# Kernel optimization log

Measured on AMD Instinct MI355X. Metric: run time of the kernel, lower is better.

## Reference

```python
import jax, jax.numpy as jnp
import numpy as np

N_NODES = 50000
N_EDGES = 800000
IN_FEATS = 512
NUM_HEADS = 4
OUT_FEATS = 64
NEG_SLOPE = 0.2


def setup_inputs() -> dict:
    key = jax.random.key(0)
    k1, k2, k3, k4, k5, k6 = jax.random.split(key, 6)
    feat = jax.random.normal(k1, (N_NODES, IN_FEATS), dtype=jnp.float32)
    W = jax.random.normal(k2, (IN_FEATS, NUM_HEADS * OUT_FEATS), dtype=jnp.float32) * (1.0 / np.sqrt(IN_FEATS))
    attn_l = jax.random.normal(k3, (NUM_HEADS, OUT_FEATS), dtype=jnp.float32) * (1.0 / np.sqrt(OUT_FEATS))
    attn_r = jax.random.normal(k4, (NUM_HEADS, OUT_FEATS), dtype=jnp.float32) * (1.0 / np.sqrt(OUT_FEATS))
    src = jax.random.randint(k5, (N_EDGES,), 0, N_NODES, dtype=jnp.int32)
    dst = jax.random.randint(k6, (N_EDGES,), 0, N_NODES, dtype=jnp.int32)
    return {"feat": feat, "W": W, "attn_l": attn_l, "attn_r": attn_r, "src": src, "dst": dst}


def reference(feat, W, attn_l, attn_r, src, dst):
    N = feat.shape[0]
    H, D = attn_l.shape
    # node-wise projection: fc(feat).view(N, H, D)
    ft = (feat @ W).reshape(N, H, D)
    # per-node attention logits
    el = jnp.einsum('nhd,hd->nh', ft, attn_l)  # [N, H]
    er = jnp.einsum('nhd,hd->nh', ft, attn_r)  # [N, H]
    # edge-wise score: leaky_relu(el[u] + er[v])
    e = jax.nn.leaky_relu(el[src] + er[dst], negative_slope=NEG_SLOPE)  # [E, H]
    # segment softmax over incoming edges of each destination node
    e_max = jax.ops.segment_max(e, dst, num_segments=N)  # [N, H]
    e_max = jnp.where(jnp.isfinite(e_max), e_max, 0.0)
    exp_e = jnp.exp(e - e_max[dst])  # [E, H]
    denom = jax.ops.segment_sum(exp_e, dst, num_segments=N)  # [N, H]
    a = exp_e / denom[dst]  # [E, H]
    # weighted message aggregation: sum_u a(u,v) * ft[u]
    msg = ft[src] * a[:, :, None]  # [E, H, D]
    out = jax.ops.segment_sum(msg, dst, num_segments=N)  # [N, H, D]
    return out.reshape(N, H * D)
```

## Files before the change

### kernel.cpp

```cpp
#include <hip/hip_runtime.h>

#define N_NODES 50000
#define N_EDGES 800000
#define IN_F    512
#define NH      4
#define DH      64
#define HD      256
#define NEG     0.2f
#define NB      ((N_NODES + 255) / 256)

typedef __attribute__((ext_vector_type(8))) short bf16x8;
typedef __attribute__((ext_vector_type(4))) float f32x4;

__device__ __forceinline__ unsigned short f2bf(float x) {
    unsigned u = __float_as_uint(x);
    unsigned r = (u + 0x7FFFu + ((u >> 16) & 1u)) >> 16;
    return (unsigned short)r;
}
__device__ __forceinline__ float bf2f(unsigned short b) {
    return __uint_as_float((unsigned)b << 16);
}

__global__ void zero_kernel(int* __restrict__ p, int n) {
    int i = blockIdx.x * blockDim.x + threadIdx.x;
    if (i < n) p[i] = 0;
}

__global__ __launch_bounds__(256) void count_kernel(const int* __restrict__ dst,
                                                    int* __restrict__ counts) {
    int e = blockIdx.x * blockDim.x + threadIdx.x;
    if (e < N_EDGES) atomicAdd(&counts[dst[e]], 1);
}

__global__ __launch_bounds__(256) void wt_kernel(const float* __restrict__ W,
                                                 unsigned short* __restrict__ Wtb) {
    int i = blockIdx.x * blockDim.x + threadIdx.x;
    if (i >= IN_F * HD) return;
    int k = i >> 8;
    int n = i & 255;
    Wtb[(size_t)n * IN_F + k] = f2bf(W[i]);
}

#define LDP 72
__global__ __launch_bounds__(256) void gemm_kernel(const float* __restrict__ A,
                                                   const unsigned short* __restrict__ Wtb,
                                                   unsigned short* __restrict__ Cb) {
    __shared__ short A_s[128][LDP];
    __shared__ short B_s[128][LDP];

    const int tid  = threadIdx.x;
    const int lane = tid & 63;
    const int wave = tid >> 6;
    const int wr   = wave >> 1;
    const int wc   = wave & 1;
    const int lm   = lane & 15;
    const int quad = lane >> 4;
    const int row0 = blockIdx.x * 128;
    const int col0 = blockIdx.y * 128;

    f32x4 acc[4][4] = {};

    for (int kt = 0; kt < IN_F; kt += 64) {
#pragma unroll
        for (int it = 0; it < 4; it++) {
            int gid = it * 256 + tid;
            int row = gid >> 3;
            int c8  = (gid & 7) * 8;
            int grow = row0 + row;
            float4 v0 = make_float4(0.f, 0.f, 0.f, 0.f);
            float4 v1 = v0;
            if (grow < N_NODES) {
                const float* ap = A + (size_t)grow * IN_F + kt + c8;
                v0 = *(const float4*)(ap);
                v1 = *(const float4*)(ap + 4);
            }
            bf16x8 s;
            s[0] = (short)f2bf(v0.x); s[1] = (short)f2bf(v0.y);
            s[2] = (short)f2bf(v0.z); s[3] = (short)f2bf(v0.w);
            s[4] = (short)f2bf(v1.x); s[5] = (short)f2bf(v1.y);
            s[6] = (short)f2bf(v1.z); s[7] = (short)f2bf(v1.w);
            *(bf16x8*)(&A_s[row][c8]) = s;
        }
#pragma unroll
        for (int it = 0; it < 4; it++) {
            int gid = it * 256 + tid;
            int row = gid >> 3;
            int c8  = (gid & 7) * 8;
            *(bf16x8*)(&B_s[row][c8]) =
                *(const bf16x8*)(Wtb + (size_t)(col0 + row) * IN_F + kt + c8);
        }
        __syncthreads();

#pragma unroll
        for (int kk = 0; kk < 64; kk += 32) {
            bf16x8 af[4], bfr[4];
#pragma unroll
            for (int i = 0; i < 4; i++)
                af[i] = *(const bf16x8*)(&A_s[wr * 64 + i * 16 + lm][kk + quad * 8]);
#pragma unroll
            for (int j = 0; j < 4; j++)
                bfr[j] = *(const bf16x8*)(&B_s[wc * 64 + j * 16 + lm][kk + quad * 8]);
#pragma unroll
            for (int i = 0; i < 4; i++)
#pragma unroll
                for (int j = 0; j < 4; j++)
                    acc[i][j] = __builtin_amdgcn_mfma_f32_16x16x32_bf16(
                        af[i], bfr[j], acc[i][j], 0, 0, 0);
        }
        __syncthreads();
    }

#pragma unroll
    for (int i = 0; i < 4; i++) {
#pragma unroll
        for (int j = 0; j < 4; j++) {
            int gcol = col0 + wc * 64 + j * 16 + lm;
#pragma unroll
            for (int r = 0; r < 4; r++) {
                int grow = row0 + wr * 64 + i * 16 + quad * 4 + r;
                if (grow < N_NODES)
                    Cb[(size_t)grow * HD + gcol] = f2bf(acc[i][j][r]);
            }
        }
    }
}

__global__ __launch_bounds__(256) void el_er_kernel(const unsigned short* __restrict__ ftb,
                                                    const float* __restrict__ attn_l,
                                                    const float* __restrict__ attn_r,
                                                    float* __restrict__ el,
                                                    float* __restrict__ er) {
    int n    = (blockIdx.x * blockDim.x + threadIdx.x) >> 6;
    int lane = threadIdx.x & 63;
    if (n >= N_NODES) return;
    int h = lane >> 4;
    int c = lane * 4;

    ushort4 fv = *(const ushort4*)(ftb + (size_t)n * HD + c);
    float4 al = *(const float4*)(attn_l + c);
    float4 ar = *(const float4*)(attn_r + c);
    float f0 = bf2f(fv.x), f1 = bf2f(fv.y), f2 = bf2f(fv.z), f3 = bf2f(fv.w);
    float pl = f0 * al.x + f1 * al.y + f2 * al.z + f3 * al.w;
    float pr = f0 * ar.x + f1 * ar.y + f2 * ar.z + f3 * ar.w;
#pragma unroll
    for (int off = 8; off > 0; off >>= 1) {
        pl += __shfl_down(pl, off);
        pr += __shfl_down(pr, off);
    }
    if ((lane & 15) == 0) {
        el[(size_t)n * NH + h] = pl;
        er[(size_t)n * NH + h] = pr;
    }
}

__global__ __launch_bounds__(256) void partial_kernel(const int* __restrict__ counts,
                                                      int* __restrict__ bsums) {
    __shared__ int red[4];
    int i = blockIdx.x * 256 + threadIdx.x;
    int c = (i < N_NODES) ? counts[i] : 0;
#pragma unroll
    for (int off = 32; off > 0; off >>= 1) c += __shfl_down(c, off);
    if ((threadIdx.x & 63) == 0) red[threadIdx.x >> 6] = c;
    __syncthreads();
    if (threadIdx.x == 0) bsums[blockIdx.x] = red[0] + red[1] + red[2] + red[3];
}

__global__ __launch_bounds__(256) void bscan_kernel(const int* __restrict__ bsums,
                                                    int* __restrict__ boffs) {
    __shared__ int s[256];
    int tid = threadIdx.x;
    s[tid] = (tid < NB) ? bsums[tid] : 0;
    __syncthreads();
    for (int off = 1; off < 256; off <<= 1) {
        int x = s[tid];
        int a = (tid >= off) ? s[tid - off] : 0;
        __syncthreads();
        s[tid] = x + a;
        __syncthreads();
    }
    if (tid < NB) boffs[tid] = (tid > 0) ? s[tid - 1] : 0;
}

__global__ __launch_bounds__(256) void scatter_scan_kernel(const int* __restrict__ counts,
                                                           const int* __restrict__ boffs,
                                                           int* __restrict__ offsets,
                                                           int* __restrict__ cursor) {
    __shared__ int s[256];
    int tid = threadIdx.x;
    int i = blockIdx.x * 256 + tid;
    s[tid] = (i < N_NODES) ? counts[i] : 0;
    __syncthreads();
    for (int off = 1; off < 256; off <<= 1) {
        int x = s[tid];
        int a = (tid >= off) ? s[tid - off] : 0;
        __syncthreads();
        s[tid] = x + a;
        __syncthreads();
    }
    int excl = (tid > 0) ? s[tid - 1] : 0;
    int o = boffs[blockIdx.x] + excl;
    if (i < N_NODES) { offsets[i] = o; cursor[i] = o; }
    if (i == 0) offsets[N_NODES] = N_EDGES;
}

__device__ __forceinline__ float lrelu_exp(float x) {
    float y = (x > 0.f) ? x : NEG * x;
    return __expf(y);
}

__global__ __launch_bounds__(256) void edge_place_kernel(const int* __restrict__ src,
                                                         const int* __restrict__ dst,
                                                         const float* __restrict__ el,
                                                         const float* __restrict__ er,
                                                         int* __restrict__ cursor,
                                                         int* __restrict__ srcs,
                                                         float* __restrict__ w4s) {
    int e = blockIdx.x * blockDim.x + threadIdx.x;
    if (e >= N_EDGES) return;
    int u = src[e], v = dst[e];
    float4 l = *(const float4*)(el + (size_t)u * NH);
    float4 r = *(const float4*)(er + (size_t)v * NH);
    float4 s;
    s.x = lrelu_exp(l.x + r.x);
    s.y = lrelu_exp(l.y + r.y);
    s.z = lrelu_exp(l.z + r.z);
    s.w = lrelu_exp(l.w + r.w);
    int pos = atomicAdd(&cursor[v], 1);
    srcs[pos] = u;
    *(float4*)(w4s + (size_t)pos * NH) = s;
}

__global__ __launch_bounds__(256) void agg_kernel(const unsigned short* __restrict__ ftb,
                                                  const float* __restrict__ w4s,
                                                  const int* __restrict__ srcs,
                                                  const int* __restrict__ offsets,
                                                  float* __restrict__ out) {
    int wv   = (blockIdx.x * blockDim.x + threadIdx.x) >> 6;
    int lane = threadIdx.x & 63;
    if (wv >= N_NODES) return;

    const int beg = offsets[wv];
    const int end = offsets[wv + 1];
    const int h   = lane >> 4;
    const size_t foff = (size_t)lane * 4;

    float4 acc = make_float4(0.f, 0.f, 0.f, 0.f);
    float dsum = 0.f;

    const int n4 = (end - beg) >> 2;
    int u0, u1, u2, u3;
    if (n4 > 0) {
        const int* sp = srcs + beg;
        u0 = sp[0]; u1 = sp[1]; u2 = sp[2]; u3 = sp[3];
        for (int b = 0; b < n4; b++) {
            const int base = beg + b * 4;
            int v0 = 0, v1 = 0, v2 = 0, v3 = 0;
            if (b + 1 < n4) {
                const int* np = srcs + base + 4;
                v0 = np[0]; v1 = np[1]; v2 = np[2]; v3 = np[3];
            }
            ushort4 f0 = *(const ushort4*)(ftb + (size_t)u0 * HD + foff);
            ushort4 f1 = *(const ushort4*)(ftb + (size_t)u1 * HD + foff);
            ushort4 f2 = *(const ushort4*)(ftb + (size_t)u2 * HD + foff);
            ushort4 f3 = *(const ushort4*)(ftb + (size_t)u3 * HD + foff);
            float w0 = w4s[(size_t)(base + 0) * NH + h];
            float w1 = w4s[(size_t)(base + 1) * NH + h];
            float w2 = w4s[(size_t)(base + 2) * NH + h];
            float w3 = w4s[(size_t)(base + 3) * NH + h];
            acc.x += w0 * bf2f(f0.x) + w1 * bf2f(f1.x) + w2 * bf2f(f2.x) + w3 * bf2f(f3.x);
            acc.y += w0 * bf2f(f0.y) + w1 * bf2f(f1.y) + w2 * bf2f(f2.y) + w3 * bf2f(f3.y);
            acc.z += w0 * bf2f(f0.z) + w1 * bf2f(f1.z) + w2 * bf2f(f2.z) + w3 * bf2f(f3.z);
            acc.w += w0 * bf2f(f0.w) + w1 * bf2f(f1.w) + w2 * bf2f(f2.w) + w3 * bf2f(f3.w);
            dsum += (w0 + w1) + (w2 + w3);
            u0 = v0; u1 = v1; u2 = v2; u3 = v3;
        }
    }
    for (int p = beg + n4 * 4; p < end; p++) {
        int u = srcs[p];
        float w = w4s[(size_t)p * NH + h];
        ushort4 f = *(const ushort4*)(ftb + (size_t)u * HD + foff);
        acc.x += w * bf2f(f.x);
        acc.y += w * bf2f(f.y);
        acc.z += w * bf2f(f.z);
        acc.w += w * bf2f(f.w);
        dsum += w;
    }

    float inv = (dsum > 0.f) ? (1.f / dsum) : 0.f;
    acc.x *= inv; acc.y *= inv; acc.z *= inv; acc.w *= inv;
    *(float4*)(out + (size_t)wv * HD + foff) = acc;
}

extern "C" void kernel_launch(void* const* d_in, const int* in_sizes, int n_in,
                              void* d_out, int out_size, void* d_ws, size_t ws_size,
                              hipStream_t stream) {
    const float* feat   = (const float*)d_in[0];
    const float* W      = (const float*)d_in[1];
    const float* attn_l = (const float*)d_in[2];
    const float* attn_r = (const float*)d_in[3];
    const int*   src    = (const int*)d_in[4];
    const int*   dst    = (const int*)d_in[5];
    float* out = (float*)d_out;

    char* p = (char*)d_ws;
    auto alloc = [&](size_t bytes) -> char* {
        char* r = p;
        p += (bytes + 255) & ~(size_t)255;
        return r;
    };
    unsigned short* ftb     = (unsigned short*)alloc((size_t)N_NODES * HD * 2);
    unsigned short* Wtb     = (unsigned short*)alloc((size_t)IN_F * HD * 2);
    float*          el      = (float*)alloc((size_t)N_NODES * NH * 4);
    float*          er      = (float*)alloc((size_t)N_NODES * NH * 4);
    float*          w4s     = (float*)alloc((size_t)N_EDGES * NH * 4);
    int*            srcs    = (int*)alloc((size_t)N_EDGES * 4);
    int*            counts  = (int*)alloc((size_t)N_NODES * 4);
    int*            offsets = (int*)alloc((size_t)(N_NODES + 1) * 4);
    int*            cursor  = (int*)alloc((size_t)N_NODES * 4);
    int*            bsums   = (int*)alloc((size_t)NB * 4);
    int*            boffs   = (int*)alloc((size_t)NB * 4);

    zero_kernel<<<(N_NODES + 255) / 256, 256, 0, stream>>>(counts, N_NODES);
    count_kernel<<<(N_EDGES + 255) / 256, 256, 0, stream>>>(dst, counts);
    wt_kernel<<<(IN_F * HD + 255) / 256, 256, 0, stream>>>(W, Wtb);
    dim3 ggrid((N_NODES + 127) / 128, HD / 128);
    gemm_kernel<<<ggrid, 256, 0, stream>>>(feat, Wtb, ftb);
    el_er_kernel<<<(N_NODES + 3) / 4, 256, 0, stream>>>(ftb, attn_l, attn_r, el, er);
    partial_kernel<<<NB, 256, 0, stream>>>(counts, bsums);
    bscan_kernel<<<1, 256, 0, stream>>>(bsums, boffs);
    scatter_scan_kernel<<<NB, 256, 0, stream>>>(counts, boffs, offsets, cursor);
    edge_place_kernel<<<(N_EDGES + 255) / 256, 256, 0, stream>>>(src, dst, el, er,
                                                                 cursor, srcs, w4s);
    agg_kernel<<<(N_NODES + 3) / 4, 256, 0, stream>>>(ftb, w4s, srcs, offsets, out);
}
```

Baseline: 357.1 us.

## Shrink GEMM row tile to 64 and prefetch next K tile into registers

The GEMM block tile shrinks from 128x128 to 64x128, which doubles the block count to about 1564 blocks so more work is spread across the CUs. It also adds register prefetching: the global loads for the next K slice are issued after the shared-memory barrier and overlap with the current slice's MFMA work. The cost is that each row of W is reread from global memory twice as often, more registers are held per thread for the prefetch buffers, and each wave does less compute per LDS load.

Result: faster. 349.5 us (-2.1%).

```diff
diff --git a/kernel.cpp b/kernel.cpp
--- a/kernel.cpp
+++ b/kernel.cpp
@@ -41,12 +41,13 @@
     Wtb[(size_t)n * IN_F + k] = f2bf(W[i]);
 }
 
-#define LDP 72
+#define LDPA 72
+#define LDPB 72
 __global__ __launch_bounds__(256) void gemm_kernel(const float* __restrict__ A,
                                                    const unsigned short* __restrict__ Wtb,
                                                    unsigned short* __restrict__ Cb) {
-    __shared__ short A_s[128][LDP];
-    __shared__ short B_s[128][LDP];
+    __shared__ short A_s[64][LDPA];
+    __shared__ short B_s[128][LDPB];
 
     const int tid  = threadIdx.x;
     const int lane = tid & 63;
@@ -55,53 +56,70 @@
     const int wc   = wave & 1;
     const int lm   = lane & 15;
     const int quad = lane >> 4;
-    const int row0 = blockIdx.x * 128;
+    const int row0 = blockIdx.x * 64;
     const int col0 = blockIdx.y * 128;
 
-    f32x4 acc[4][4] = {};
+    const int srow = tid >> 3;
+    const int sc8  = (tid & 7) * 8;
+
+    f32x4 acc[2][4] = {};
+    float4 pa[4];
+    bf16x8 pb[4];
+
+#define LOAD_TILES(KT)                                                         \
+    {                                                                          \
+        int g0 = row0 + srow;                                                  \
+        if (g0 < N_NODES) {                                                    \
+            const float* ap = A + (size_t)g0 * IN_F + (KT) + sc8;              \
+            pa[0] = *(const float4*)ap; pa[1] = *(const float4*)(ap + 4);      \
+        } else { pa[0] = pa[1] = make_float4(0.f, 0.f, 0.f, 0.f); }            \
+        int g1 = row0 + 32 + srow;                                             \
+        if (g1 < N_NODES) {                                                    \
+            const float* ap = A + (size_t)g1 * IN_F + (KT) + sc8;              \
+            pa[2] = *(const float4*)ap; pa[3] = *(const float4*)(ap + 4);      \
+        } else { pa[2] = pa[3] = make_float4(0.f, 0.f, 0.f, 0.f); }            \
+        _Pragma("unroll")                                                      \
+        for (int it = 0; it < 4; it++) {                                       \
+            int brow = it * 32 + srow;                                         \
+            pb[it] = *(const bf16x8*)(Wtb + (size_t)(col0 + brow) * IN_F +     \
+                                      (KT) + sc8);                             \
+        }                                                                      \
+    }
+
+    LOAD_TILES(0);
 
     for (int kt = 0; kt < IN_F; kt += 64) {
-#pragma unroll
-        for (int it = 0; it < 4; it++) {
-            int gid = it * 256 + tid;
-            int row = gid >> 3;
-            int c8  = (gid & 7) * 8;
-            int grow = row0 + row;
-            float4 v0 = make_float4(0.f, 0.f, 0.f, 0.f);
-            float4 v1 = v0;
-            if (grow < N_NODES) {
-                const float* ap = A + (size_t)grow * IN_F + kt + c8;
-                v0 = *(const float4*)(ap);
-                v1 = *(const float4*)(ap + 4);
-            }
+        {
             bf16x8 s;
-            s[0] = (short)f2bf(v0.x); s[1] = (short)f2bf(v0.y);
-            s[2] = (short)f2bf(v0.z); s[3] = (short)f2bf(v0.w);
-            s[4] = (short)f2bf(v1.x); s[5] = (short)f2bf(v1.y);
-            s[6] = (short)f2bf(v1.z); s[7] = (short)f2bf(v1.w);
-            *(bf16x8*)(&A_s[row][c8]) = s;
+            s[0] = (short)f2bf(pa[0].x); s[1] = (short)f2bf(pa[0].y);
+            s[2] = (short)f2bf(pa[0].z); s[3] = (short)f2bf(pa[0].w);
+            s[4] = (short)f2bf(pa[1].x); s[5] = (short)f2bf(pa[1].y);
+            s[6] = (short)f2bf(pa[1].z); s[7] = (short)f2bf(pa[1].w);
+            *(bf16x8*)(&A_s[srow][sc8]) = s;
+            s[0] = (short)f2bf(pa[2].x); s[1] = (short)f2bf(pa[2].y);
+            s[2] = (short)f2bf(pa[2].z); s[3] = (short)f2bf(pa[2].w);
+            s[4] = (short)f2bf(pa[3].x); s[5] = (short)f2bf(pa[3].y);
+            s[6] = (short)f2bf(pa[3].z); s[7] = (short)f2bf(pa[3].w);
+            *(bf16x8*)(&A_s[32 + srow][sc8]) = s;
+#pragma unroll
+            for (int it = 0; it < 4; it++)
+                *(bf16x8*)(&B_s[it * 32 + srow][sc8]) = pb[it];
         }
-#pragma unroll
-        for (int it = 0; it < 4; it++) {
-            int gid = it * 256 + tid;
-            int row = gid >> 3;
-            int c8  = (gid & 7) * 8;
-            *(bf16x8*)(&B_s[row][c8]) =
-                *(const bf16x8*)(Wtb + (size_t)(col0 + row) * IN_F + kt + c8);
-        }
-        __syncthreads();
+        __syncthreads();
+
+        if (kt + 64 < IN_F) LOAD_TILES(kt + 64);
 
 #pragma unroll
         for (int kk = 0; kk < 64; kk += 32) {
-            bf16x8 af[4], bfr[4];
-#pragma unroll
-            for (int i = 0; i < 4; i++)
-                af[i] = *(const bf16x8*)(&A_s[wr * 64 + i * 16 + lm][kk + quad * 8]);
+            bf16x8 af[2], bfr[4];
+#pragma unroll
+            for (int i = 0; i < 2; i++)
+                af[i] = *(const bf16x8*)(&A_s[wr * 32 + i * 16 + lm][kk + quad * 8]);
 #pragma unroll
             for (int j = 0; j < 4; j++)
                 bfr[j] = *(const bf16x8*)(&B_s[wc * 64 + j * 16 + lm][kk + quad * 8]);
 #pragma unroll
-            for (int i = 0; i < 4; i++)
+            for (int i = 0; i < 2; i++)
 #pragma unroll
                 for (int j = 0; j < 4; j++)
                     acc[i][j] = __builtin_amdgcn_mfma_f32_16x16x32_bf16(
@@ -109,15 +127,16 @@
         }
         __syncthreads();
     }
-
-#pragma unroll
-    for (int i = 0; i < 4; i++) {
+#undef LOAD_TILES
+
+#pragma unroll
+    for (int i = 0; i < 2; i++) {
 #pragma unroll
         for (int j = 0; j < 4; j++) {
             int gcol = col0 + wc * 64 + j * 16 + lm;
 #pragma unroll
             for (int r = 0; r < 4; r++) {
-                int grow = row0 + wr * 64 + i * 16 + quad * 4 + r;
+                int grow = row0 + wr * 32 + i * 16 + quad * 4 + r;
                 if (grow < N_NODES)
                     Cb[(size_t)grow * HD + gcol] = f2bf(acc[i][j][r]);
             }
@@ -323,7 +342,7 @@
     zero_kernel<<<(N_NODES + 255) / 256, 256, 0, stream>>>(counts, N_NODES);
     count_kernel<<<(N_EDGES + 255) / 256, 256, 0, stream>>>(dst, counts);
     wt_kernel<<<(IN_F * HD + 255) / 256, 256, 0, stream>>>(W, Wtb);
-    dim3 ggrid((N_NODES + 127) / 128, HD / 128);
+    dim3 ggrid((N_NODES + 63) / 64, HD / 128);
     gemm_kernel<<<ggrid, 256, 0, stream>>>(feat, Wtb, ftb);
     el_er_kernel<<<(N_NODES + 3) / 4, 256, 0, stream>>>(ftb, attn_l, attn_r, el, er);
     partial_kernel<<<NB, 256, 0, stream>>>(counts, bsums);
```
